# Optimization experiments

Hardware: AMD Instinct MI355X
Metric: run time of the kernel (lower is better)

## Reference

```python
import jax, jax.numpy as jnp
import numpy as np

N_NODES, N_EDGES = 16000, 256000
M_IN_S, M_IN_V = 16, 8   # input irreps: 16x0e + 8x1o (dim 40)
M_K_S, M_K_V = 8, 4      # key/query irreps: 8x0e + 4x1o
M_V_S, M_V_V = 16, 8     # value irreps: 16x0e + 8x1o
NUM_BASIS, R_CUT = 32, 2.5
SQ3 = 1.7320508075688772  # sqrt(3)


def _fc_net(r, W1, W2):
    # e3nn FullyConnectedNet([num_basis,16,numels], silu): weight-normalized linears
    h = jax.nn.silu(r @ (W1 / jnp.sqrt(jnp.float32(W1.shape[0]))))
    return h @ (W2 / jnp.sqrt(jnp.float32(W2.shape[0])))


def _edge_tp(xs, xv, y0, y1, w, m1s, m1v, mos, mov):
    # FullyConnectedTensorProduct(in1 = m1s x0e + m1v x1o, in2 = 1x0e + 1x1o,
    #   out = mos x0e + mov x1o), per-edge external weights w [E, numels].
    # Paths: 0e*0e->0e, 1o*1o->0e (dot/sqrt3), 0e*1o->1o, 1o*0e->1o.
    E = w.shape[0]
    n1, n2, n3 = m1s * mos, m1v * mos, m1s * mov
    w_ss = w[:, :n1].reshape(E, m1s, mos)
    w_vv = w[:, n1:n1 + n2].reshape(E, m1v, mos)
    w_sv = w[:, n1 + n2:n1 + n2 + n3].reshape(E, m1s, mov)
    w_vs = w[:, n1 + n2 + n3:].reshape(E, m1v, mov)
    inv = 1.0 / jnp.sqrt(jnp.float32(m1s + m1v))  # fan-in path normalization
    out_s = (jnp.einsum('ei,eio->eo', xs * y0[:, None], w_ss)
             + jnp.einsum('eic,ec,eio->eo', xv, y1, w_vv) / SQ3) * inv
    out_v = (jnp.einsum('ei,ec,eio->eoc', xs, y1, w_sv)
             + jnp.einsum('eic,eio->eoc', xv * y0[:, None, None], w_vs)) * inv
    return out_s, out_v


def _forward(pos, x, Wq_s, Wq_v, Wk1, Wk2, Wv1, Wv2, Ws_ss, Ws_vv, edge_src, edge_dst):
    xs, xv = x[:, :M_IN_S], x[:, M_IN_S:].reshape(-1, M_IN_V, 3)
    vec = pos[edge_dst] - pos[edge_src]                       # [E,3]
    d = jnp.linalg.norm(vec, axis=1)
    d_safe = jnp.maximum(d, 1e-6)
    # bessel radial basis with cutoff (soft_one_hot_linspace, basis='bessel') * sqrt(num_basis)
    n = jnp.arange(1, NUM_BASIS + 1, dtype=jnp.float32)
    rad = jnp.sqrt(2.0 / R_CUT) * jnp.sin(n[None] * jnp.pi * d_safe[:, None] / R_CUT) / d_safe[:, None]
    rad = jnp.where((d < R_CUT)[:, None], rad, 0.0) * jnp.sqrt(jnp.float32(NUM_BASIS))
    # spherical harmonics lmax=1, normalize=True, component normalization
    vh = vec / d_safe[:, None]
    y0, y1 = jnp.ones_like(d), SQ3 * vh
    # query projection (o3.Linear: per-irrep linear with 1/sqrt(fan_in))
    q_s = xs @ Wq_s / jnp.sqrt(jnp.float32(M_IN_S))           # [N, M_K_S]
    q_v = jnp.einsum('nic,io->noc', xv, Wq_v) / jnp.sqrt(jnp.float32(M_IN_V))
    # per-edge tensor-product weights from radial MLPs (shared_weights=False)
    wk = _fc_net(rad, Wk1, Wk2)                               # [E, 288]
    wv = _fc_net(rad, Wv1, Wv2)                               # [E, 576]
    xs_e, xv_e = xs[edge_src], xv[edge_src]
    k_s, k_v = _edge_tp(xs_e, xv_e, y0, y1, wk, M_IN_S, M_IN_V, M_K_S, M_K_V)
    v_s, v_v = _edge_tp(xs_e, xv_e, y0, y1, wv, M_IN_S, M_IN_V, M_V_S, M_V_V)
    # similarity tensor product (query x key -> 0e), shared internal weights
    fan = jnp.sqrt(jnp.float32(M_K_S * M_K_S + M_K_V * M_K_V))
    sim = (jnp.einsum('ei,ij,ej->e', q_s[edge_dst], Ws_ss, k_s)
           + jnp.einsum('eic,ij,ejc->e', q_v[edge_dst], Ws_vv, k_v) / SQ3) / fan
    # scatter softmax over incoming edges of each dst node
    attn = jnp.exp(sim)
    Z = jax.ops.segment_sum(attn, edge_dst, num_segments=N_NODES)
    a = attn / Z[edge_dst]
    # weighted scatter-sum aggregation
    out_s = jax.ops.segment_sum(a[:, None] * v_s, edge_dst, num_segments=N_NODES)
    out_v = jax.ops.segment_sum(a[:, None, None] * v_v, edge_dst, num_segments=N_NODES)
    return jnp.concatenate([out_s, out_v.reshape(N_NODES, -1)], axis=1)  # [N, 40]


def setup_inputs() -> dict:
    key = jax.random.key(0)
    ks = jax.random.split(key, 12)
    wk_numels = M_IN_S * M_K_S + M_IN_V * M_K_S + M_IN_S * M_K_V + M_IN_V * M_K_V  # 288
    wv_numels = M_IN_S * M_V_S + M_IN_V * M_V_S + M_IN_S * M_V_V + M_IN_V * M_V_V  # 576
    return {
        'pos': jax.random.uniform(ks[0], (N_NODES, 3), jnp.float32) * 3.0,
        'x': jax.random.normal(ks[1], (N_NODES, M_IN_S + 3 * M_IN_V), jnp.float32),
        'Wq_s': jax.random.normal(ks[2], (M_IN_S, M_K_S), jnp.float32),
        'Wq_v': jax.random.normal(ks[3], (M_IN_V, M_K_V), jnp.float32),
        'Wk1': jax.random.normal(ks[4], (NUM_BASIS, 16), jnp.float32),
        'Wk2': jax.random.normal(ks[5], (16, wk_numels), jnp.float32),
        'Wv1': jax.random.normal(ks[6], (NUM_BASIS, 16), jnp.float32),
        'Wv2': jax.random.normal(ks[7], (16, wv_numels), jnp.float32),
        'Ws_ss': jax.random.normal(ks[8], (M_K_S, M_K_S), jnp.float32) * 0.1,
        'Ws_vv': jax.random.normal(ks[9], (M_K_V, M_K_V), jnp.float32) * 0.1,
        'edge_src': jax.random.randint(ks[10], (N_EDGES,), 0, N_NODES),
        'edge_dst': jax.random.randint(ks[11], (N_EDGES,), 0, N_NODES),
    }


def reference(pos, x, Wq_s, Wq_v, Wk1, Wk2, Wv1, Wv2, Ws_ss, Ws_vv, edge_src, edge_dst):
    return _forward(pos, x, Wq_s, Wq_v, Wk1, Wk2, Wv1, Wv2, Ws_ss, Ws_vv, edge_src, edge_dst)
```

## Files before the change

### kernel.cpp

```cpp
#include <hip/hip_runtime.h>
#include <hip/hip_bf16.h>

#define N_NODES 16000
#define N_EDGES 256000

#define OFF_SD     0
#define OFF_SIMB   512000
#define OFF_CNT    768000
#define OFF_START  784000
#define OFF_CUR    800001
#define OFF_WB     816004
#define OFF_WBK    834436
#define OFF_QT     846724
#define OFF_Z      1006724
#define OFF_GT     1022724

typedef _Float16 f16x2 __attribute__((ext_vector_type(2)));
typedef _Float16 f16x8v __attribute__((ext_vector_type(8)));
typedef float f32x4v __attribute__((ext_vector_type(4)));

__device__ __forceinline__ float fdot2f(f16x2 a, f16x2 b, float c) {
#if __has_builtin(__builtin_amdgcn_fdot2)
  return __builtin_amdgcn_fdot2(a, b, c, false);
#else
  return fmaf((float)a.x, (float)b.x, fmaf((float)a.y, (float)b.y, c));
#endif
}

__device__ __forceinline__ unsigned packh2(float a, float b) {
  union { unsigned u; f16x2 p; } v;
  v.p.x = (_Float16)a; v.p.y = (_Float16)b;
  return v.u;
}

__device__ __forceinline__ unsigned splat_half(unsigned x, unsigned sel) {
#if __has_builtin(__builtin_amdgcn_perm)
  return __builtin_amdgcn_perm(x, x, sel);
#else
  unsigned h = (sel == 0x03020302u) ? (x >> 16) : (x & 0xffffu);
  return h | (h << 16);
#endif
}

__device__ __forceinline__ void gload_lds16(const unsigned* g, unsigned* l) {
#if __has_builtin(__builtin_amdgcn_global_load_lds)
  __builtin_amdgcn_global_load_lds((const __attribute__((address_space(1))) unsigned*)g,
                                   (__attribute__((address_space(3))) unsigned*)l, 16, 0, 0);
#else
  *(uint4*)l = *(const uint4*)g;
#endif
}

__device__ __forceinline__ void load_row40(const float* __restrict__ p, float* xr) {
  const float4* rp = reinterpret_cast<const float4*>(p);
#pragma unroll
  for (int q = 0; q < 10; ++q) {
    float4 f = rp[q];
    xr[4 * q + 0] = f.x; xr[4 * q + 1] = f.y; xr[4 * q + 2] = f.z; xr[4 * q + 3] = f.w;
  }
}

struct EdgeGeom { float vhx, vhy, vhz, y1x, y1y, y1z; };

__device__ __forceinline__ void edge_h_pk(const float* __restrict__ pos, int s, int d,
                                          const unsigned* W1, f16x2* hp, EdgeGeom& g) {
  float vx = pos[3 * d + 0] - pos[3 * s + 0];
  float vy = pos[3 * d + 1] - pos[3 * s + 1];
  float vz = pos[3 * d + 2] - pos[3 * s + 2];
  float dist = sqrtf(fmaf(vx, vx, fmaf(vy, vy, vz * vz)));
  float dsafe = fmaxf(dist, 1e-6f);
  float rinv = 1.0f / dsafe;
  g.vhx = vx * rinv; g.vhy = vy * rinv; g.vhz = vz * rinv;
  g.y1x = 1.7320508075688772f * g.vhx;
  g.y1y = 1.7320508075688772f * g.vhy;
  g.y1z = 1.7320508075688772f * g.vhz;
  float pre[16];
#pragma unroll
  for (int t = 0; t < 16; ++t) pre[t] = 0.f;
  float sx, cx;
  sincosf(1.2566370614359172f * dsafe, &sx, &cx);
  cx = fminf(1.f, fmaxf(-1.f, cx));
  float twoc = 2.f * cx;
  float sprev = 0.f, scur = sx;
  float rscale = (dist < 2.5f) ? (5.059644256269407f * rinv) : 0.f;
#pragma unroll
  for (int bp = 0; bp < 16; ++bp) {
    float r0 = rscale * scur;
    float sn = fmaf(twoc, scur, -sprev); sprev = scur; scur = sn;
    float r1 = rscale * scur;
    sn = fmaf(twoc, scur, -sprev); sprev = scur; scur = sn;
    union { unsigned u; f16x2 p; } rp; rp.p.x = (_Float16)r0; rp.p.y = (_Float16)r1;
    union { uint4 u[4]; f16x2 p[16]; } w;
    w.u[0] = *(const uint4*)(W1 + bp * 16);
    w.u[1] = *(const uint4*)(W1 + bp * 16 + 4);
    w.u[2] = *(const uint4*)(W1 + bp * 16 + 8);
    w.u[3] = *(const uint4*)(W1 + bp * 16 + 12);
#pragma unroll
    for (int t = 0; t < 16; ++t) pre[t] = fdot2f(rp.p, w.p[t], pre[t]);
  }
#pragma unroll
  for (int tp = 0; tp < 8; ++tp) {
    float h0 = pre[2 * tp]     / (1.f + __expf(-pre[2 * tp]));
    float h1 = pre[2 * tp + 1] / (1.f + __expf(-pre[2 * tp + 1]));
    hp[tp].x = (_Float16)h0; hp[tp].y = (_Float16)h1;
  }
}

__global__ void k_hist(const int* __restrict__ edst, int* __restrict__ cnt) {
  int e = blockIdx.x * 256 + threadIdx.x;
  atomicAdd(&cnt[edst[e]], 1);
}

__global__ void k_scan2(const int* __restrict__ cnt, int* __restrict__ cur,
                        int* __restrict__ gtot) {
  int n = blockIdx.x * 256 + threadIdx.x;
  if (n < N_NODES) cur[n] = atomicAdd(gtot, cnt[n]);
}

__global__ void k_fill(const int* __restrict__ esrc, const int* __restrict__ edst,
                       int* __restrict__ cur, int2* __restrict__ sd) {
  int e = blockIdx.x * 256 + threadIdx.x;
  int d = edst[e];
  int slot = atomicAdd(&cur[d], 1);
  sd[slot] = make_int2(esrc[e], d);
}

#define PREP_ZERO_B   2626
#define PREP_PB_B     144
#define PREP_PBK_B    96
#define PREP_NQ_B     63
#define PREP_TOTAL_B  (PREP_ZERO_B + PREP_PB_B + PREP_PBK_B + PREP_NQ_B)

__global__ void __launch_bounds__(256) k_prep(
    const float* __restrict__ x,
    const float* __restrict__ Wq_s, const float* __restrict__ Wq_v,
    const float* __restrict__ Wss, const float* __restrict__ Wvv,
    const float* __restrict__ Wk2, const float* __restrict__ Wv2,
    int* __restrict__ cnt, float* __restrict__ Z, float* __restrict__ out,
    unsigned short* __restrict__ WB, unsigned short* __restrict__ WBK,
    unsigned short* __restrict__ QT, int* __restrict__ gtot) {
  int b = blockIdx.x;
  if (b < PREP_ZERO_B) {
    int i = b * 256 + threadIdx.x;
    if (i < 16000)       cnt[i] = 0;
    else if (i < 32000)  Z[i - 16000] = 0.f;
    else if (i < 672000) out[i - 32000] = 0.f;
    else if (i == 672000) *gtot = 0;
    return;
  }
  b -= PREP_ZERO_B;
  if (b < PREP_PB_B) {
    int idx = b * 256 + threadIdx.x;
    int j = idx & 7;
    int lane = (idx >> 3) & 63;
    int t3 = idx >> 9;
    int ct = t3 % 3, kk = t3 / 3;
    int q = lane >> 4, m = lane & 15;
    int row = 32 * kk + 8 * q + j;
    int col = 16 * ct + m;
    int t = row & 15;
    float v = 0.f;
    if (row < 256) {
      int i = row >> 4;
      if (col < 16)      v = Wv2[t * 576 + i * 16 + col];
      else if (col < 24) v = Wv2[t * 576 + 384 + i * 8 + (col - 16)];
    } else if (row < 384) {
      int i = (row - 256) >> 4;
      if (col < 16)      v = Wv2[t * 576 + 256 + i * 16 + col];
    } else {
      int part = (row - 384) >> 7;
      int i = ((row - 384) & 127) >> 4;
      int cb = 24 + 8 * part;
      if (col >= cb && col < cb + 8) v = Wv2[t * 576 + 512 + i * 8 + (col - cb)];
    }
    union { unsigned short u; _Float16 h; } cv;
    cv.h = (_Float16)(v * 0.051031036307982884f);
    WB[idx] = cv.u;
    return;
  }
  b -= PREP_PB_B;
  if (b < PREP_PBK_B) {
    int idx = b * 256 + threadIdx.x;
    int j = idx & 7;
    int lane = (idx >> 3) & 63;
    int t2 = idx >> 9;
    int ct = t2 & 1, kk = t2 >> 1;
    int q = lane >> 4, m = lane & 15;
    int row = 32 * kk + 8 * q + j;
    int col = 16 * ct + m;
    int t = row & 15;
    float v = 0.f;
    if (col < 24) {
      if (row < 256) {
        int i = row >> 4;
        if (col < 8)       v = Wk2[t * 288 + i * 8 + col];
        else if (col < 12) v = Wk2[t * 288 + 192 + i * 4 + (col - 8)];
      } else if (row < 384) {
        int i = (row - 256) >> 4;
        if (col < 8)       v = Wk2[t * 288 + 128 + i * 8 + col];
      } else {
        int c = (row - 384) >> 7;
        int i = ((row - 384) & 127) >> 4;
        int cb = 12 + 4 * c;
        if (col >= cb && col < cb + 4) v = Wk2[t * 288 + 256 + i * 4 + (col - cb)];
      }
    }
    union { unsigned short u; _Float16 h; } cv;
    cv.h = (_Float16)(v * 0.051031036307982884f);
    WBK[idx] = cv.u;
    return;
  }
  b -= PREP_PBK_B;
  __shared__ float Ls[240];
  if (threadIdx.x < 240) {
    int i = threadIdx.x;
    float v;
    if (i < 128)      v = Wq_s[i] * 0.25f;
    else if (i < 160) v = Wq_v[i - 128] * 0.3535533905932738f;
    else if (i < 224) v = Wss[i - 160] * 0.11180339887498948f;
    else              v = Wvv[i - 224] * 0.06454972243679028f;
    Ls[i] = v;
  }
  __syncthreads();
  int n = b * 256 + threadIdx.x;
  if (n >= N_NODES) return;
  float xd[40];
  load_row40(x + 40 * n, xd);
  float qd[8], qvd[12];
#pragma unroll
  for (int o = 0; o < 8; ++o) qd[o] = 0.f;
#pragma unroll
  for (int i = 0; i < 16; ++i)
#pragma unroll
    for (int o = 0; o < 8; ++o) qd[o] = fmaf(xd[i], Ls[8 * i + o], qd[o]);
#pragma unroll
  for (int k = 0; k < 12; ++k) qvd[k] = 0.f;
#pragma unroll
  for (int i = 0; i < 8; ++i)
#pragma unroll
    for (int o = 0; o < 4; ++o)
#pragma unroll
      for (int c = 0; c < 3; ++c)
        qvd[3 * o + c] = fmaf(xd[16 + 3 * i + c], Ls[128 + 4 * i + o], qvd[3 * o + c]);
  float qf[20];
#pragma unroll
  for (int j = 0; j < 8; ++j) {
    float t = 0.f;
#pragma unroll
    for (int i = 0; i < 8; ++i) t = fmaf(qd[i], Ls[160 + 8 * i + j], t);
    qf[j] = t;
  }
#pragma unroll
  for (int o = 0; o < 4; ++o)
#pragma unroll
    for (int c = 0; c < 3; ++c) {
      float t = 0.f;
#pragma unroll
      for (int i = 0; i < 4; ++i) t = fmaf(qvd[3 * i + c], Ls[224 + 4 * i + o], t);
      qf[8 + 3 * o + c] = t;
    }
  uint2* qp = (uint2*)(QT + 20 * n);
#pragma unroll
  for (int bq = 0; bq < 5; ++bq) {
    uint2 st;
    st.x = packh2(qf[4 * bq], qf[4 * bq + 1]);
    st.y = packh2(qf[4 * bq + 2], qf[4 * bq + 3]);
    qp[bq] = st;
  }
}

#define RSTR 36

__device__ __forceinline__ void build_coef(const float* xr, const float* Bv, float* coef) {
#pragma unroll
  for (int i = 0; i < 16; ++i) coef[i] = xr[i];
#pragma unroll
  for (int i = 0; i < 8; ++i) coef[16 + i] = Bv[i];
#pragma unroll
  for (int p = 0; p < 4; ++p)
#pragma unroll
    for (int c = 0; c < 3; ++c) {
      coef[24 + 8 * c + 2 * p]     = xr[16 + 6 * p + c];
      coef[24 + 8 * c + 2 * p + 1] = xr[16 + 6 * p + 3 + c];
    }
}

__global__ void __launch_bounds__(256) k_edge1(
    const float* __restrict__ pos, const float* __restrict__ x,
    const float* __restrict__ Wk1, const unsigned short* __restrict__ WBK,
    const unsigned short* __restrict__ QT,
    const int2* __restrict__ sd, float* __restrict__ simb, float* __restrict__ Z) {
  __shared__ __align__(16) unsigned LW1[256];
  __shared__ __align__(16) unsigned SM[4][64 * RSTR];
  __shared__ __align__(16) unsigned BB[2][2048];

  {
    int i = threadIdx.x;
    int bp = i >> 4, t = i & 15;
    LW1[i] = packh2(Wk1[(2 * bp) * 16 + t] * 0.17677669529663687f,
                    Wk1[(2 * bp + 1) * 16 + t] * 0.17677669529663687f);
  }
  __syncthreads();

  int wave = threadIdx.x >> 6, lane = threadIdx.x & 63;
  int q = lane >> 4, m = lane & 15;
  int q1 = q & 1;
  unsigned seld = (q >> 1) ? 0x03020302u : 0x01000100u;
  int slot = blockIdx.x * 256 + threadIdx.x;
  int2 e = sd[slot];
  int s = e.x, d = e.y;

  f16x2 hp[8]; EdgeGeom g;
  edge_h_pk(pos, s, d, LW1, hp, g);

  float qf[20];
  {
    const uint2* qp = (const uint2*)(QT + 20 * d);
#pragma unroll
    for (int b = 0; b < 5; ++b) {
      uint2 u = qp[b];
      union { unsigned d; f16x2 p; } a0, a1;
      a0.d = u.x; a1.d = u.y;
      qf[4 * b] = (float)a0.p.x; qf[4 * b + 1] = (float)a0.p.y;
      qf[4 * b + 2] = (float)a1.p.x; qf[4 * b + 3] = (float)a1.p.y;
    }
  }

  float xr[40];
  load_row40(x + 40 * s, xr);
  float Bv[8];
#pragma unroll
  for (int i = 0; i < 8; ++i)
    Bv[i] = fmaf(xr[16 + 3 * i], g.vhx, fmaf(xr[17 + 3 * i], g.vhy, xr[18 + 3 * i] * g.vhz));
  float coef[48];
  build_coef(xr, Bv, coef);

  unsigned* row = &SM[wave][lane * RSTR];
  {
    union { uint4 u; f16x2 p[4]; } h0, h1;
#pragma unroll
    for (int k = 0; k < 4; ++k) { h0.p[k] = hp[k]; h1.p[k] = hp[4 + k]; }
    *(uint4*)(row) = h0.u;
    *(uint4*)(row + 4) = h1.u;
  }
#pragma unroll
  for (int bt = 0; bt < 6; ++bt) {
    uint4 w;
    w.x = packh2(coef[8 * bt + 0], coef[8 * bt + 1]);
    w.y = packh2(coef[8 * bt + 2], coef[8 * bt + 3]);
    w.z = packh2(coef[8 * bt + 4], coef[8 * bt + 5]);
    w.w = packh2(coef[8 * bt + 6], coef[8 * bt + 7]);
    *(uint4*)(row + 8 + 4 * bt) = w;
  }
  unsigned* wbase = &SM[wave][0];
  union { uint4 u; f16x2 p[4]; } hs[4];
#pragma unroll
  for (int rt = 0; rt < 4; ++rt)
    hs[rt].u = *(const uint4*)(wbase + (16 * rt + m) * RSTR + 4 * q1);

  const uint4* WBq = (const uint4*)WBK;
  f32x4v acc[4][2];
#pragma unroll
  for (int rt = 0; rt < 4; ++rt)
#pragma unroll
    for (int ct = 0; ct < 2; ++ct) { f32x4v z = {0.f, 0.f, 0.f, 0.f}; acc[rt][ct] = z; }

#pragma unroll
  for (int j = 0; j < 2; ++j)
    gload_lds16((const unsigned*)(WBq + j * 256 + threadIdx.x),
                &BB[0][(j * 256 + threadIdx.x) * 4]);
  __syncthreads();

#pragma unroll
  for (int bt = 0; bt < 6; ++bt) {
    if (bt < 5) {
#pragma unroll
      for (int j = 0; j < 2; ++j)
        gload_lds16((const unsigned*)(WBq + (bt + 1) * 512 + j * 256 + threadIdx.x),
                    &BB[(bt + 1) & 1][(j * 256 + threadIdx.x) * 4]);
    }
    union { uint4 u; unsigned d[4]; } cb[4];
#pragma unroll
    for (int rt = 0; rt < 4; ++rt)
      cb[rt].u = *(const uint4*)(wbase + (16 * rt + m) * RSTR + 8 + 4 * bt);
    const uint4* Bq = (const uint4*)BB[bt & 1];
#pragma unroll
    for (int t = 0; t < 4; ++t) {
      union { uint4 u; f16x2 p[4]; f16x8v v; } av[4];
#pragma unroll
      for (int rt = 0; rt < 4; ++rt) {
        union { unsigned d; f16x2 p; } sp;
        sp.d = splat_half(cb[rt].d[t], seld);
#pragma unroll
        for (int w = 0; w < 4; ++w) av[rt].p[w] = hs[rt].p[w] * sp.p;
      }
#pragma unroll
      for (int ct = 0; ct < 2; ++ct) {
        union { uint4 u; f16x8v v; } bf;
        bf.u = Bq[(t * 2 + ct) * 64 + lane];
#pragma unroll
        for (int rt = 0; rt < 4; ++rt)
          acc[rt][ct] = __builtin_amdgcn_mfma_f32_16x16x32_f16(av[rt].v, bf.v, acc[rt][ct], 0, 0, 0);
      }
    }
    __syncthreads();
  }

  float P[24];
  float* ctb = (float*)wbase;
#pragma unroll
  for (int rt = 0; rt < 4; ++rt)
#pragma unroll
    for (int r = 0; r < 4; ++r)
      ctb[m * 65 + 16 * rt + 4 * q + r] = acc[rt][0][r];
#pragma unroll
  for (int o = 0; o < 16; ++o) P[o] = ctb[o * 65 + lane];
#pragma unroll
  for (int rt = 0; rt < 4; ++rt)
#pragma unroll
    for (int r = 0; r < 4; ++r)
      ctb[m * 65 + 16 * rt + 4 * q + r] = acc[rt][1][r];
#pragma unroll
  for (int o = 0; o < 8; ++o) P[16 + o] = ctb[o * 65 + lane];

  float sim = 0.f;
#pragma unroll
  for (int j = 0; j < 8; ++j) sim = fmaf(qf[j], P[j], sim);
  float y1c[3] = {g.y1x, g.y1y, g.y1z};
#pragma unroll
  for (int o = 0; o < 4; ++o)
#pragma unroll
    for (int c = 0; c < 3; ++c)
      sim = fmaf(qf[8 + 3 * o + c], fmaf(y1c[c], P[8 + o], P[12 + 4 * c + o]), sim);

  float ev = __expf(sim);
  simb[slot] = ev;
  bool same[6];
#pragma unroll
  for (int k = 0; k < 6; ++k) {
    int dd = __shfl_down(d, 1 << k, 64);
    same[k] = ((lane + (1 << k)) < 64) && (dd == d);
  }
  int dprev = __shfl_up(d, 1, 64);
  bool head = (lane == 0) || (dprev != d);
  float v = ev;
#pragma unroll
  for (int k = 0; k < 6; ++k) {
    float ov = __shfl_down(v, 1 << k, 64);
    v += same[k] ? ov : 0.f;
  }
  if (head) atomicAdd(&Z[d], v);
}

__global__ void __launch_bounds__(256) k_edge2(
    const float* __restrict__ pos, const float* __restrict__ x,
    const float* __restrict__ Wv1, const unsigned short* __restrict__ WB,
    const int2* __restrict__ sd, const float* __restrict__ eb,
    const float* __restrict__ Zv, float* __restrict__ out) {
  __shared__ __align__(16) unsigned LW1[256];
  __shared__ __align__(16) unsigned SM[4][64 * RSTR];
  __shared__ __align__(16) unsigned BB[2][3072];

  {
    int i = threadIdx.x;
    int bp = i >> 4, t = i & 15;
    LW1[i] = packh2(Wv1[(2 * bp) * 16 + t] * 0.17677669529663687f,
                    Wv1[(2 * bp + 1) * 16 + t] * 0.17677669529663687f);
  }
  __syncthreads();

  int wave = threadIdx.x >> 6, lane = threadIdx.x & 63;
  int q = lane >> 4, m = lane & 15;
  int q1 = q & 1;
  unsigned seld = (q >> 1) ? 0x03020302u : 0x01000100u;
  int slot = blockIdx.x * 256 + threadIdx.x;
  int2 e = sd[slot];
  int s = e.x, d = e.y;

  float ev = eb[slot];
  float Zd = Zv[d];

  bool same[6];
#pragma unroll
  for (int k = 0; k < 6; ++k) {
    int dd = __shfl_down(d, 1 << k, 64);
    same[k] = ((lane + (1 << k)) < 64) && (dd == d);
  }
  int dprev = __shfl_up(d, 1, 64);
  bool head = (lane == 0) || (dprev != d);

  f16x2 hp[8]; EdgeGeom g;
  edge_h_pk(pos, s, d, LW1, hp, g);
  float xr[40];
  load_row40(x + 40 * s, xr);
  float Bv[8];
#pragma unroll
  for (int i = 0; i < 8; ++i)
    Bv[i] = fmaf(xr[16 + 3 * i], g.vhx, fmaf(xr[17 + 3 * i], g.vhy, xr[18 + 3 * i] * g.vhz));
  float coef[48];
  build_coef(xr, Bv, coef);
  float a = ev / Zd;

  unsigned* row = &SM[wave][lane * RSTR];
  {
    union { uint4 u; f16x2 p[4]; } h0, h1;
#pragma unroll
    for (int k = 0; k < 4; ++k) { h0.p[k] = hp[k]; h1.p[k] = hp[4 + k]; }
    *(uint4*)(row) = h0.u;
    *(uint4*)(row + 4) = h1.u;
  }
#pragma unroll
  for (int bt = 0; bt < 6; ++bt) {
    uint4 w;
    w.x = packh2(coef[8 * bt + 0], coef[8 * bt + 1]);
    w.y = packh2(coef[8 * bt + 2], coef[8 * bt + 3]);
    w.z = packh2(coef[8 * bt + 4], coef[8 * bt + 5]);
    w.w = packh2(coef[8 * bt + 6], coef[8 * bt + 7]);
    *(uint4*)(row + 8 + 4 * bt) = w;
  }
  unsigned* wbase = &SM[wave][0];
  union { uint4 u; f16x2 p[4]; } hs[4];
#pragma unroll
  for (int rt = 0; rt < 4; ++rt)
    hs[rt].u = *(const uint4*)(wbase + (16 * rt + m) * RSTR + 4 * q1);

  const uint4* WBq = (const uint4*)WB;
  f32x4v acc[4][3];
#pragma unroll
  for (int rt = 0; rt < 4; ++rt)
#pragma unroll
    for (int ct = 0; ct < 3; ++ct) { f32x4v z = {0.f, 0.f, 0.f, 0.f}; acc[rt][ct] = z; }

#pragma unroll
  for (int j = 0; j < 3; ++j)
    gload_lds16((const unsigned*)(WBq + j * 256 + threadIdx.x),
                &BB[0][(j * 256 + threadIdx.x) * 4]);
  __syncthreads();

#pragma unroll
  for (int bt = 0; bt < 6; ++bt) {
    if (bt < 5) {
#pragma unroll
      for (int j = 0; j < 3; ++j)
        gload_lds16((const unsigned*)(WBq + (bt + 1) * 768 + j * 256 + threadIdx.x),
                    &BB[(bt + 1) & 1][(j * 256 + threadIdx.x) * 4]);
    }
    union { uint4 u; unsigned d[4]; } cb[4];
#pragma unroll
    for (int rt = 0; rt < 4; ++rt)
      cb[rt].u = *(const uint4*)(wbase + (16 * rt + m) * RSTR + 8 + 4 * bt);
    const uint4* Bq = (const uint4*)BB[bt & 1];
#pragma unroll
    for (int t = 0; t < 4; ++t) {
      union { uint4 u; f16x2 p[4]; f16x8v v; } av[4];
#pragma unroll
      for (int rt = 0; rt < 4; ++rt) {
        union { unsigned d; f16x2 p; } sp;
        sp.d = splat_half(cb[rt].d[t], seld);
#pragma unroll
        for (int w = 0; w < 4; ++w) av[rt].p[w] = hs[rt].p[w] * sp.p;
      }
#pragma unroll
      for (int ct = 0; ct < 3; ++ct) {
        union { uint4 u; f16x8v v; } bf;
        bf.u = Bq[(t * 3 + ct) * 64 + lane];
#pragma unroll
        for (int rt = 0; rt < 4; ++rt)
          acc[rt][ct] = __builtin_amdgcn_mfma_f32_16x16x32_f16(av[rt].v, bf.v, acc[rt][ct], 0, 0, 0);
      }
    }
    __syncthreads();
  }

  float* ctb = (float*)wbase;
  float* op = out + 40 * d;

  {
#pragma unroll
    for (int rt = 0; rt < 4; ++rt)
#pragma unroll
      for (int r = 0; r < 4; ++r)
        ctb[m * 65 + 16 * rt + 4 * q + r] = acc[rt][0][r];
    float P0[16];
#pragma unroll
    for (int o = 0; o < 16; ++o) P0[o] = ctb[o * 65 + lane];
#pragma unroll
    for (int o = 0; o < 16; ++o) {
      float v = a * P0[o];
#pragma unroll
      for (int k = 0; k < 6; ++k) {
        float ov = __shfl_down(v, 1 << k, 64);
        v += same[k] ? ov : 0.f;
      }
      if (head) atomicAdd(op + o, v);
    }
  }
  float P1[16], P2[16];
#pragma unroll
  for (int rt = 0; rt < 4; ++rt)
#pragma unroll
    for (int r = 0; r < 4; ++r)
      ctb[m * 65 + 16 * rt + 4 * q + r] = acc[rt][1][r];
#pragma unroll
  for (int o = 0; o < 16; ++o) P1[o] = ctb[o * 65 + lane];
#pragma unroll
  for (int rt = 0; rt < 4; ++rt)
#pragma unroll
    for (int r = 0; r < 4; ++r)
      ctb[m * 65 + 16 * rt + 4 * q + r] = acc[rt][2][r];
#pragma unroll
  for (int o = 0; o < 16; ++o) P2[o] = ctb[o * 65 + lane];
#pragma unroll
  for (int o = 0; o < 8; ++o) {
    float s1v = P1[o];
    float vc[3];
    vc[0] = a * fmaf(g.y1x, s1v, P1[8 + o]);
    vc[1] = a * fmaf(g.y1y, s1v, P2[o]);
    vc[2] = a * fmaf(g.y1z, s1v, P2[8 + o]);
#pragma unroll
    for (int c = 0; c < 3; ++c) {
      float v = vc[c];
#pragma unroll
      for (int k = 0; k < 6; ++k) {
        float ov = __shfl_down(v, 1 << k, 64);
        v += same[k] ? ov : 0.f;
      }
      if (head) atomicAdd(op + 16 + 3 * o + c, v);
    }
  }
}

extern "C" void kernel_launch(void* const* d_in, const int* in_sizes, int n_in,
                              void* d_out, int out_size, void* d_ws, size_t ws_size,
                              hipStream_t stream) {
  (void)in_sizes; (void)n_in; (void)out_size; (void)ws_size;
  const float* pos  = (const float*)d_in[0];
  const float* x    = (const float*)d_in[1];
  const float* Wq_s = (const float*)d_in[2];
  const float* Wq_v = (const float*)d_in[3];
  const float* Wk1  = (const float*)d_in[4];
  const float* Wk2  = (const float*)d_in[5];
  const float* Wv1  = (const float*)d_in[6];
  const float* Wv2  = (const float*)d_in[7];
  const float* Wss  = (const float*)d_in[8];
  const float* Wvv  = (const float*)d_in[9];
  const int* esrc = (const int*)d_in[10];
  const int* edst = (const int*)d_in[11];
  int*   wsi  = (int*)d_ws;
  float* wsf  = (float*)d_ws;
  float* out  = (float*)d_out;

  int2*  sd    = (int2*)(wsi + OFF_SD);
  float* simb  = wsf + OFF_SIMB;
  int*   cnt   = wsi + OFF_CNT;
  int*   cur   = wsi + OFF_CUR;
  unsigned short* WB  = (unsigned short*)(wsf + OFF_WB);
  unsigned short* WBK = (unsigned short*)(wsf + OFF_WBK);
  unsigned short* QT  = (unsigned short*)(wsf + OFF_QT);
  float* Z    = wsf + OFF_Z;
  int*   gtot = wsi + OFF_GT;

  k_prep<<<PREP_TOTAL_B, 256, 0, stream>>>(x, Wq_s, Wq_v, Wss, Wvv, Wk2, Wv2,
                                           cnt, Z, out, WB, WBK, QT, gtot);
  k_hist<<<1000, 256, 0, stream>>>(edst, cnt);
  k_scan2<<<63, 256, 0, stream>>>(cnt, cur, gtot);
  k_fill<<<1000, 256, 0, stream>>>(esrc, edst, cur, sd);
  k_edge1<<<1000, 256, 0, stream>>>(pos, x, Wk1, WBK, QT, sd, simb, Z);
  k_edge2<<<1000, 256, 0, stream>>>(pos, x, Wv1, WB, sd, simb, Z, out);
}
```

Before: 201.9 us.

## Drop destination-sort of edges and scatter with per-edge atomics directly

```diff
diff --git a/kernel.cpp b/kernel.cpp
--- a/kernel.cpp
+++ b/kernel.cpp
@@ -4,16 +4,11 @@
 #define N_NODES 16000
 #define N_EDGES 256000
 
-#define OFF_SD     0
 #define OFF_SIMB   512000
-#define OFF_CNT    768000
-#define OFF_START  784000
-#define OFF_CUR    800001
 #define OFF_WB     816004
 #define OFF_WBK    834436
 #define OFF_QT     846724
 #define OFF_Z      1006724
-#define OFF_GT     1022724
 
 typedef _Float16 f16x2 __attribute__((ext_vector_type(2)));
 typedef _Float16 f16x8v __attribute__((ext_vector_type(8)));
@@ -106,26 +101,7 @@
   }
 }
 
-__global__ void k_hist(const int* __restrict__ edst, int* __restrict__ cnt) {
-  int e = blockIdx.x * 256 + threadIdx.x;
-  atomicAdd(&cnt[edst[e]], 1);
-}
-
-__global__ void k_scan2(const int* __restrict__ cnt, int* __restrict__ cur,
-                        int* __restrict__ gtot) {
-  int n = blockIdx.x * 256 + threadIdx.x;
-  if (n < N_NODES) cur[n] = atomicAdd(gtot, cnt[n]);
-}
-
-__global__ void k_fill(const int* __restrict__ esrc, const int* __restrict__ edst,
-                       int* __restrict__ cur, int2* __restrict__ sd) {
-  int e = blockIdx.x * 256 + threadIdx.x;
-  int d = edst[e];
-  int slot = atomicAdd(&cur[d], 1);
-  sd[slot] = make_int2(esrc[e], d);
-}
-
-#define PREP_ZERO_B   2626
+#define PREP_ZERO_B   2563
 #define PREP_PB_B     144
 #define PREP_PBK_B    96
 #define PREP_NQ_B     63
@@ -136,16 +112,14 @@
     const float* __restrict__ Wq_s, const float* __restrict__ Wq_v,
     const float* __restrict__ Wss, const float* __restrict__ Wvv,
     const float* __restrict__ Wk2, const float* __restrict__ Wv2,
-    int* __restrict__ cnt, float* __restrict__ Z, float* __restrict__ out,
+    float* __restrict__ Z, float* __restrict__ out,
     unsigned short* __restrict__ WB, unsigned short* __restrict__ WBK,
-    unsigned short* __restrict__ QT, int* __restrict__ gtot) {
+    unsigned short* __restrict__ QT) {
   int b = blockIdx.x;
   if (b < PREP_ZERO_B) {
     int i = b * 256 + threadIdx.x;
-    if (i < 16000)       cnt[i] = 0;
-    else if (i < 32000)  Z[i - 16000] = 0.f;
-    else if (i < 672000) out[i - 32000] = 0.f;
-    else if (i == 672000) *gtot = 0;
+    if (i < 16000)       Z[i] = 0.f;
+    else if (i < 656000) out[i - 16000] = 0.f;
     return;
   }
   b -= PREP_ZERO_B;
@@ -289,10 +263,14 @@
     const float* __restrict__ pos, const float* __restrict__ x,
     const float* __restrict__ Wk1, const unsigned short* __restrict__ WBK,
     const unsigned short* __restrict__ QT,
-    const int2* __restrict__ sd, float* __restrict__ simb, float* __restrict__ Z) {
+    const int* __restrict__ esrc, const int* __restrict__ edst,
+    float* __restrict__ simb, float* __restrict__ Z) {
   __shared__ __align__(16) unsigned LW1[256];
   __shared__ __align__(16) unsigned SM[4][64 * RSTR];
   __shared__ __align__(16) unsigned BB[2][2048];
+
+  int e = blockIdx.x * 256 + threadIdx.x;
+  int s = esrc[e], d = edst[e];
 
   {
     int i = threadIdx.x;
@@ -306,9 +284,6 @@
   int q = lane >> 4, m = lane & 15;
   int q1 = q & 1;
   unsigned seld = (q >> 1) ? 0x03020302u : 0x01000100u;
-  int slot = blockIdx.x * 256 + threadIdx.x;
-  int2 e = sd[slot];
-  int s = e.x, d = e.y;
 
   f16x2 hp[8]; EdgeGeom g;
   edge_h_pk(pos, s, d, LW1, hp, g);
@@ -434,32 +409,25 @@
       sim = fmaf(qf[8 + 3 * o + c], fmaf(y1c[c], P[8 + o], P[12 + 4 * c + o]), sim);
 
   float ev = __expf(sim);
-  simb[slot] = ev;
-  bool same[6];
-#pragma unroll
-  for (int k = 0; k < 6; ++k) {
-    int dd = __shfl_down(d, 1 << k, 64);
-    same[k] = ((lane + (1 << k)) < 64) && (dd == d);
-  }
-  int dprev = __shfl_up(d, 1, 64);
-  bool head = (lane == 0) || (dprev != d);
-  float v = ev;
-#pragma unroll
-  for (int k = 0; k < 6; ++k) {
-    float ov = __shfl_down(v, 1 << k, 64);
-    v += same[k] ? ov : 0.f;
-  }
-  if (head) atomicAdd(&Z[d], v);
+  simb[e] = ev;
+  atomicAdd(&Z[d], ev);
 }
 
 __global__ void __launch_bounds__(256) k_edge2(
     const float* __restrict__ pos, const float* __restrict__ x,
     const float* __restrict__ Wv1, const unsigned short* __restrict__ WB,
-    const int2* __restrict__ sd, const float* __restrict__ eb,
-    const float* __restrict__ Zv, float* __restrict__ out) {
+    const int* __restrict__ esrc, const int* __restrict__ edst,
+    const float* __restrict__ eb, const float* __restrict__ Zv,
+    float* __restrict__ out) {
   __shared__ __align__(16) unsigned LW1[256];
   __shared__ __align__(16) unsigned SM[4][64 * RSTR];
   __shared__ __align__(16) unsigned BB[2][3072];
+
+  int e = blockIdx.x * 256 + threadIdx.x;
+  int s = esrc[e], d = edst[e];
+
+  float ev = eb[e];
+  float Zd = Zv[d];
 
   {
     int i = threadIdx.x;
@@ -473,21 +441,6 @@
   int q = lane >> 4, m = lane & 15;
   int q1 = q & 1;
   unsigned seld = (q >> 1) ? 0x03020302u : 0x01000100u;
-  int slot = blockIdx.x * 256 + threadIdx.x;
-  int2 e = sd[slot];
-  int s = e.x, d = e.y;
-
-  float ev = eb[slot];
-  float Zd = Zv[d];
-
-  bool same[6];
-#pragma unroll
-  for (int k = 0; k < 6; ++k) {
-    int dd = __shfl_down(d, 1 << k, 64);
-    same[k] = ((lane + (1 << k)) < 64) && (dd == d);
-  }
-  int dprev = __shfl_up(d, 1, 64);
-  bool head = (lane == 0) || (dprev != d);
 
   f16x2 hp[8]; EdgeGeom g;
   edge_h_pk(pos, s, d, LW1, hp, g);
@@ -585,15 +538,7 @@
 #pragma unroll
     for (int o = 0; o < 16; ++o) P0[o] = ctb[o * 65 + lane];
 #pragma unroll
-    for (int o = 0; o < 16; ++o) {
-      float v = a * P0[o];
-#pragma unroll
-      for (int k = 0; k < 6; ++k) {
-        float ov = __shfl_down(v, 1 << k, 64);
-        v += same[k] ? ov : 0.f;
-      }
-      if (head) atomicAdd(op + o, v);
-    }
+    for (int o = 0; o < 16; ++o) atomicAdd(op + o, a * P0[o]);
   }
   float P1[16], P2[16];
 #pragma unroll
@@ -613,20 +558,9 @@
 #pragma unroll
   for (int o = 0; o < 8; ++o) {
     float s1v = P1[o];
-    float vc[3];
-    vc[0] = a * fmaf(g.y1x, s1v, P1[8 + o]);
-    vc[1] = a * fmaf(g.y1y, s1v, P2[o]);
-    vc[2] = a * fmaf(g.y1z, s1v, P2[8 + o]);
-#pragma unroll
-    for (int c = 0; c < 3; ++c) {
-      float v = vc[c];
-#pragma unroll
-      for (int k = 0; k < 6; ++k) {
-        float ov = __shfl_down(v, 1 << k, 64);
-        v += same[k] ? ov : 0.f;
-      }
-      if (head) atomicAdd(op + 16 + 3 * o + c, v);
-    }
+    atomicAdd(op + 16 + 3 * o + 0, a * fmaf(g.y1x, s1v, P1[8 + o]));
+    atomicAdd(op + 16 + 3 * o + 1, a * fmaf(g.y1y, s1v, P2[o]));
+    atomicAdd(op + 16 + 3 * o + 2, a * fmaf(g.y1z, s1v, P2[8 + o]));
   }
 }
 
@@ -646,25 +580,17 @@
   const float* Wvv  = (const float*)d_in[9];
   const int* esrc = (const int*)d_in[10];
   const int* edst = (const int*)d_in[11];
-  int*   wsi  = (int*)d_ws;
   float* wsf  = (float*)d_ws;
   float* out  = (float*)d_out;
 
-  int2*  sd    = (int2*)(wsi + OFF_SD);
   float* simb  = wsf + OFF_SIMB;
-  int*   cnt   = wsi + OFF_CNT;
-  int*   cur   = wsi + OFF_CUR;
   unsigned short* WB  = (unsigned short*)(wsf + OFF_WB);
   unsigned short* WBK = (unsigned short*)(wsf + OFF_WBK);
   unsigned short* QT  = (unsigned short*)(wsf + OFF_QT);
   float* Z    = wsf + OFF_Z;
-  int*   gtot = wsi + OFF_GT;
 
   k_prep<<<PREP_TOTAL_B, 256, 0, stream>>>(x, Wq_s, Wq_v, Wss, Wvv, Wk2, Wv2,
-                                           cnt, Z, out, WB, WBK, QT, gtot);
-  k_hist<<<1000, 256, 0, stream>>>(edst, cnt);
-  k_scan2<<<63, 256, 0, stream>>>(cnt, cur, gtot);
-  k_fill<<<1000, 256, 0, stream>>>(esrc, edst, cur, sd);
-  k_edge1<<<1000, 256, 0, stream>>>(pos, x, Wk1, WBK, QT, sd, simb, Z);
-  k_edge2<<<1000, 256, 0, stream>>>(pos, x, Wv1, WB, sd, simb, Z, out);
-}
+                                           Z, out, WB, WBK, QT);
+  k_edge1<<<1000, 256, 0, stream>>>(pos, x, Wk1, WBK, QT, esrc, edst, simb, Z);
+  k_edge2<<<1000, 256, 0, stream>>>(pos, x, Wv1, WB, esrc, edst, simb, Z, out);
+}
```

New measurement: 653.9 us. 224% more time.
